# Optimization experiments

Measured on AMD Instinct MI355X. Metric: run time of the kernel, lower is better.

The kernel has to match this reference:

```python
import jax, jax.numpy as jnp
import numpy as np

H = 200
W = 200
SH = 2.0  # h / h_meters = 200/100
SW = 2.0
THRESH = 0.05   # opacity prune threshold
CHUNK = 128     # gaussians per scan step
EPS_T = 1e-4    # 3DGS transmittance early-stop
ALPHA_MIN = 1.0 / 255.0


def _rasterize(means3D, colors, opac, cov3D):
    """Orthographic BEV 3D-Gaussian-splat rasterization for one sample.
    means3D (N,3), colors (N,d), opac (N,1), cov3D (N,6) packed [xx,xy,xz,yy,yz,zz].
    Returns (d, H, W) image. Depth is identically 0 under the BEV view matrix,
    so compositing order is the input order (stable), matching the CUDA sort.
    """
    N, d = colors.shape
    P = H * W
    # pixel centers, row-major flatten: p = y*W + x
    gy, gx = jnp.meshgrid(jnp.arange(H, dtype=jnp.float32),
                          jnp.arange(W, dtype=jnp.float32), indexing='ij')
    pxf = gx.reshape(-1)
    pyf = gy.reshape(-1)

    # project means with full_proj_transform: u = -sh*y + H/2, v = -sw*x + W/2
    u = -SH * means3D[:, 1] + H / 2.0
    v = -SW * means3D[:, 0] + W / 2.0

    # 2D covariance: W2 @ Cov3D @ W2^T + 0.3*I with W2 = [[0,sh,0],[sw,0,0]]
    a = SH * SH * cov3D[:, 3] + 0.3   # var along image x (from Sigma_yy)
    c = SW * SW * cov3D[:, 0] + 0.3   # var along image y (from Sigma_xx)
    b = SH * SW * cov3D[:, 1]
    det = a * c - b * b
    valid = det > 0.0
    det_s = jnp.where(valid, det, 1.0)
    conA = c / det_s
    conB = b / det_s   # power uses +conB*dx*dy (conic.y = -b/det in CUDA)
    conC = a / det_s

    # fold pruning mask (opacity threshold) and validity into opacity
    op = jnp.where((opac[:, 0] > THRESH) & valid, opac[:, 0], 0.0)

    K = N // CHUNK
    chunks = tuple(t.reshape(K, CHUNK, *t.shape[1:])
                   for t in (u, v, conA, conB, conC, op, colors))

    def body(carry, ch):
        img, T = carry  # img (P,d), T (P,)
        u_, v_, A_, B_, C_, op_, col_ = ch
        dx = u_[:, None] - pxf[None, :]          # (C,P)
        dy = v_[:, None] - pyf[None, :]
        power = -0.5 * (A_[:, None] * dx * dx + C_[:, None] * dy * dy) \
                + B_[:, None] * dx * dy
        alpha = jnp.minimum(0.99, op_[:, None] * jnp.exp(jnp.minimum(power, 0.0)))
        # CUDA skips power>0 and alpha < 1/255
        alpha = jnp.where((power > 0.0) | (alpha < ALPHA_MIN), 0.0, alpha)
        # early termination: skip gaussian i (and all after) once T would drop < 1e-4
        T_incl = T[None, :] * jnp.cumprod(1.0 - alpha, axis=0)
        alpha = jnp.where(T_incl < EPS_T, 0.0, alpha)
        cp = jnp.cumprod(1.0 - alpha, axis=0)    # inclusive products
        T_excl = jnp.concatenate([jnp.ones((1, P), dtype=cp.dtype), cp[:-1]], axis=0)
        wgt = alpha * T_excl * T[None, :]        # (C,P)
        img = img + jnp.einsum('cp,cd->pd', wgt, col_)
        T = T * cp[-1]
        return (img, T), None

    img0 = jnp.zeros((P, d), dtype=colors.dtype)
    T0 = jnp.ones((P,), dtype=colors.dtype)
    (img, T), _ = jax.lax.scan(body, (img0, T0), chunks)
    # background is zeros -> no bg term; reshape to (d, H, W)
    return img.reshape(H, W, d).transpose(2, 0, 1)


def setup_inputs() -> dict:
    key = jax.random.key(0)
    k1, k2, k3, k4 = jax.random.split(key, 4)
    B, N, D = 2, 1024, 32
    features = jax.random.normal(k1, (B, N, D), dtype=jnp.float32)
    # BEV covers +/-50m; scale positions so most gaussians land on the canvas
    means3D = jax.random.normal(k2, (B, N, 3), dtype=jnp.float32) * 20.0
    cov3D = jax.random.uniform(k3, (B, N, 6), dtype=jnp.float32)
    opacities = jax.random.uniform(k4, (B, N, 1), dtype=jnp.float32)
    return {"features": features, "means3D": means3D,
            "cov3D": cov3D, "opacities": opacities}


def reference(features, means3D, cov3D, opacities):
    bev = jax.vmap(_rasterize)(means3D, features, opacities, cov3D)  # (B,d,H,W)
    mask = opacities[..., 0] > THRESH
    mean_count = mask.astype(jnp.float32).sum(axis=1).mean()
    return bev, mean_count
```

## Files before the change

### kernel.cpp

```cpp
#include <hip/hip_runtime.h>


#define HH 200
#define WW 200
#define DD 32
#define NG 1024
#define BB 2
#define OUT_IMG (BB*DD*HH*WW)
#define NW 4
#define SEGG (NG/NW)
#define NGRP (SEGG/64)

__global__ __launch_bounds__(64*NW) void render_kernel(
    const float* __restrict__ feats,
    const float* __restrict__ means,
    const float* __restrict__ cov,
    const float* __restrict__ opac,
    float* __restrict__ out)
{
    __shared__ float su[NW][64], sv[NW][64], sA[NW][64], sB[NW][64],
                     sC[NW][64], sop[NW][64], spl[NW][64];
    __shared__ int   sg[NW][64];
    __shared__ float4 simg[NW][64][8];
    __shared__ float sT[NW][64];
    __shared__ float wsum[NW];

    const int b    = blockIdx.z;
    const int tid  = threadIdx.x;
    const int lane = tid & 63;
    const int wid  = tid >> 6;
    const int px   = blockIdx.x*8 + (lane & 7);
    const int py   = blockIdx.y*8 + (lane >> 3);
    const float pxf = (float)px, pyf = (float)py;
    const float cx  = blockIdx.x*8 + 3.5f;
    const float cy  = blockIdx.y*8 + 3.5f;

    const float* __restrict__ featsB = feats + (size_t)b * NG * DD;
    const int gB = b * NG;

    float4 acc[8];
#pragma unroll
    for (int j = 0; j < 8; ++j) acc[j] = make_float4(0.f,0.f,0.f,0.f);
    float T = 1.f, P = 1.f;
    bool skip = false;

    for (int k = 0; k < NGRP; ++k) {
        const int gl = wid*SEGG + k*64 + lane;
        const int g  = gB + gl;
        const float o  = opac[g];
        const float c0 = cov[g*6+0], c1 = cov[g*6+1], c3 = cov[g*6+3];
        const float av = 4.f*c3 + 0.3f;
        const float cv = 4.f*c0 + 0.3f;
        const float bv = 4.f*c1;
        const float det = av*cv - bv*bv;
        bool flag = false;
        float u=0.f, v=0.f, A=0.f, Bc=0.f, Cc=0.f, pl=0.f;
        if (o > 0.05f && det > 0.f) {
            const float inv = 1.f/det;
            A = cv*inv; Bc = bv*inv; Cc = av*inv;
            u = -2.f*means[g*3+1] + 100.f;
            v = -2.f*means[g*3+0] + 100.f;
            pl = -__logf(255.f*o);
            const float qmax = -2.f*pl;
            const float htr = 0.5f*(A+Cc), hdf = 0.5f*(A-Cc);
            const float lmin = htr - sqrtf(hdf*hdf + Bc*Bc);
            const float r = sqrtf(qmax/lmin) + 0.5f;
            flag = (fabsf(u - cx) <= 3.5f + r) && (fabsf(v - cy) <= 3.5f + r);
        }
        const unsigned long long mask = __ballot(flag);
        const int m = (int)__popcll(mask);
        __syncthreads();
        if (flag) {
            const int pos = (int)__popcll(mask & ((1ull << lane) - 1ull));
            su[wid][pos]=u;  sv[wid][pos]=v;  sA[wid][pos]=A;  sB[wid][pos]=Bc;
            sC[wid][pos]=Cc; sop[wid][pos]=o; spl[wid][pos]=pl; sg[wid][pos]=gl;
        }
        __syncthreads();

        if (!skip) {
            for (int i = 0; i < m; ++i) {
                const float dx = su[wid][i] - pxf;
                const float dy = sv[wid][i] - pyf;
                const float pw = fmaf(sB[wid][i], dx*dy,
                                      -0.5f*(sA[wid][i]*dx*dx + sC[wid][i]*dy*dy));
                if (pw > 0.f) continue;
                if (pw < spl[wid][i] - 1e-3f) continue;
                const float alpha = fminf(0.99f, sop[wid][i] * __expf(pw));
                if (alpha < (1.f/255.f)) continue;
                const float om = 1.f - alpha;
                const float tp = T * P;
                if (tp * om < 1e-4f) { skip = true; break; }
                const float w = alpha * tp;
                const float4* __restrict__ col =
                    (const float4*)(featsB + (size_t)sg[wid][i] * DD);
#pragma unroll
                for (int j = 0; j < 8; ++j) {
                    const float4 c4 = col[j];
                    acc[j].x = fmaf(w, c4.x, acc[j].x);
                    acc[j].y = fmaf(w, c4.y, acc[j].y);
                    acc[j].z = fmaf(w, c4.z, acc[j].z);
                    acc[j].w = fmaf(w, c4.w, acc[j].w);
                }
                P *= om;
            }
        }
        if (k & 1) { T *= P; P = 1.f; skip = false; }
    }

    sT[wid][lane] = T;
#pragma unroll
    for (int j = 0; j < 8; ++j)
        simg[wid][lane][(j + lane) & 7] = acc[j];
    __syncthreads();

    {
        const int p   = tid & 63;
        const int grp = tid >> 6;
        const float t0 = sT[0][p], t1 = sT[1][p], t2 = sT[2][p];
        const float pf1 = t0, pf2 = t0*t1, pf3 = pf2*t2;
        const int ppx = blockIdx.x*8 + (p & 7);
        const int ppy = blockIdx.y*8 + (p >> 3);
        const size_t base = (size_t)b * DD * (HH*WW) + (size_t)ppy * WW + ppx;
#pragma unroll
        for (int q = 0; q < 2; ++q) {
            const int c4 = grp*2 + q;
            const int slot = (c4 + p) & 7;
            const float4 r0 = simg[0][p][slot];
            const float4 r1 = simg[1][p][slot];
            const float4 r2 = simg[2][p][slot];
            const float4 r3 = simg[3][p][slot];
            float4 ov;
            ov.x = fmaf(pf3, r3.x, fmaf(pf2, r2.x, fmaf(pf1, r1.x, r0.x)));
            ov.y = fmaf(pf3, r3.y, fmaf(pf2, r2.y, fmaf(pf1, r1.y, r0.y)));
            ov.z = fmaf(pf3, r3.z, fmaf(pf2, r2.z, fmaf(pf1, r1.z, r0.z)));
            ov.w = fmaf(pf3, r3.w, fmaf(pf2, r2.w, fmaf(pf1, r1.w, r0.w)));
            out[base + (size_t)(c4*4+0)*(HH*WW)] = ov.x;
            out[base + (size_t)(c4*4+1)*(HH*WW)] = ov.y;
            out[base + (size_t)(c4*4+2)*(HH*WW)] = ov.z;
            out[base + (size_t)(c4*4+3)*(HH*WW)] = ov.w;
        }
    }

    if (blockIdx.x == 0 && blockIdx.y == 0 && b == 0) {
        float s = 0.f;
        for (int i = tid; i < BB*NG; i += 64*NW)
            s += (opac[i] > 0.05f) ? 1.f : 0.f;
#pragma unroll
        for (int off = 32; off > 0; off >>= 1)
            s += __shfl_down(s, off, 64);
        if (lane == 0) wsum[wid] = s;
        __syncthreads();
        if (tid == 0)
            out[OUT_IMG] = (wsum[0]+wsum[1]+wsum[2]+wsum[3]) * (1.f/(float)BB);
    }
}

extern "C" void kernel_launch(void* const* d_in, const int* in_sizes, int n_in,
                              void* d_out, int out_size, void* d_ws, size_t ws_size,
                              hipStream_t stream) {
    const float* feats = (const float*)d_in[0];
    const float* means = (const float*)d_in[1];
    const float* cvr   = (const float*)d_in[2];
    const float* opc   = (const float*)d_in[3];
    float* out = (float*)d_out;

    render_kernel<<<dim3(WW/8, HH/8, BB), dim3(64*NW), 0, stream>>>(
        feats, means, cvr, opc, out);
}
```

Before: 77.47 us.

## Split gaussians across eight waves per tile and merge with tree reduction

Each 8x8 pixel tile now uses eight wavefronts instead of four, so each wave handles 128 gaussians. That halves the serial compositing loop per wave. The per-wave partial images are combined front-to-back through a three-level shared-memory tree reduction that carries the transmittance products. Per-pair early termination is replaced by a per-wave running transmittance, and the gaussian index is made wave-uniform with readfirstlane so the color loads can use scalar addressing. In exchange, blocks get larger, there are more barriers, and early termination within a wave's segment no longer sees the transmittance from earlier waves, so wasted work can grow.

```diff
diff --git a/kernel.cpp b/kernel.cpp
--- a/kernel.cpp
+++ b/kernel.cpp
@@ -7,7 +7,7 @@
 #define NG 1024
 #define BB 2
 #define OUT_IMG (BB*DD*HH*WW)
-#define NW 4
+#define NW 8
 #define SEGG (NG/NW)
 #define NGRP (SEGG/64)
 
@@ -20,10 +20,10 @@
 {
     __shared__ float su[NW][64], sv[NW][64], sA[NW][64], sB[NW][64],
                      sC[NW][64], sop[NW][64], spl[NW][64];
-    __shared__ int   sg[NW][64];
-    __shared__ float4 simg[NW][64][8];
-    __shared__ float sT[NW][64];
-    __shared__ float wsum[NW];
+    __shared__ int   sg_[NW][64];
+    __shared__ float4 slab[4][64][8];
+    __shared__ float  slabT[4][64];
+    __shared__ float  wsum[NW];
 
     const int b    = blockIdx.z;
     const int tid  = threadIdx.x;
@@ -41,7 +41,7 @@
     float4 acc[8];
 #pragma unroll
     for (int j = 0; j < 8; ++j) acc[j] = make_float4(0.f,0.f,0.f,0.f);
-    float T = 1.f, P = 1.f;
+    float T = 1.f;
     bool skip = false;
 
     for (int k = 0; k < NGRP; ++k) {
@@ -73,7 +73,7 @@
         if (flag) {
             const int pos = (int)__popcll(mask & ((1ull << lane) - 1ull));
             su[wid][pos]=u;  sv[wid][pos]=v;  sA[wid][pos]=A;  sB[wid][pos]=Bc;
-            sC[wid][pos]=Cc; sop[wid][pos]=o; spl[wid][pos]=pl; sg[wid][pos]=gl;
+            sC[wid][pos]=Cc; sop[wid][pos]=o; spl[wid][pos]=pl; sg_[wid][pos]=gl;
         }
         __syncthreads();
 
@@ -88,11 +88,11 @@
                 const float alpha = fminf(0.99f, sop[wid][i] * __expf(pw));
                 if (alpha < (1.f/255.f)) continue;
                 const float om = 1.f - alpha;
-                const float tp = T * P;
-                if (tp * om < 1e-4f) { skip = true; break; }
-                const float w = alpha * tp;
+                if (T * om < 1e-4f) { skip = true; break; }
+                const float w = alpha * T;
+                const int gi = __builtin_amdgcn_readfirstlane(sg_[wid][i]);
                 const float4* __restrict__ col =
-                    (const float4*)(featsB + (size_t)sg[wid][i] * DD);
+                    (const float4*)(featsB + (size_t)gi * DD);
 #pragma unroll
                 for (int j = 0; j < 8; ++j) {
                     const float4 c4 = col[j];
@@ -101,44 +101,56 @@
                     acc[j].z = fmaf(w, c4.z, acc[j].z);
                     acc[j].w = fmaf(w, c4.w, acc[j].w);
                 }
-                P *= om;
+                T *= om;
             }
         }
-        if (k & 1) { T *= P; P = 1.f; skip = false; }
     }
 
-    sT[wid][lane] = T;
+    float Tl = T;
 #pragma unroll
-    for (int j = 0; j < 8; ++j)
-        simg[wid][lane][(j + lane) & 7] = acc[j];
+    for (int phase = 0; phase < 3; ++phase) {
+        const int step = 1 << phase;
+        const int mod  = 2*step - 1;
+        const bool storer = (wid & mod) == step;
+        const bool merger = (wid & mod) == 0 && wid + step < NW;
+        __syncthreads();
+        if (storer) {
+            const int s = wid >> (phase+1);
+#pragma unroll
+            for (int j = 0; j < 8; ++j)
+                slab[s][lane][(j + lane) & 7] = acc[j];
+            slabT[s][lane] = Tl;
+        }
+        __syncthreads();
+        if (merger) {
+            const int s = (wid + step) >> (phase+1);
+            const float Th = slabT[s][lane];
+#pragma unroll
+            for (int j = 0; j < 8; ++j) {
+                const float4 r = slab[s][lane][(j + lane) & 7];
+                acc[j].x = fmaf(Tl, r.x, acc[j].x);
+                acc[j].y = fmaf(Tl, r.y, acc[j].y);
+                acc[j].z = fmaf(Tl, r.z, acc[j].z);
+                acc[j].w = fmaf(Tl, r.w, acc[j].w);
+            }
+            Tl *= Th;
+        }
+    }
+
     __syncthreads();
-
+    if (wid == 0) {
+#pragma unroll
+        for (int j = 0; j < 8; ++j)
+            slab[0][lane][(j + lane) & 7] = acc[j];
+    }
+    __syncthreads();
     {
-        const int p   = tid & 63;
-        const int grp = tid >> 6;
-        const float t0 = sT[0][p], t1 = sT[1][p], t2 = sT[2][p];
-        const float pf1 = t0, pf2 = t0*t1, pf3 = pf2*t2;
-        const int ppx = blockIdx.x*8 + (p & 7);
-        const int ppy = blockIdx.y*8 + (p >> 3);
-        const size_t base = (size_t)b * DD * (HH*WW) + (size_t)ppy * WW + ppx;
-#pragma unroll
-        for (int q = 0; q < 2; ++q) {
-            const int c4 = grp*2 + q;
-            const int slot = (c4 + p) & 7;
-            const float4 r0 = simg[0][p][slot];
-            const float4 r1 = simg[1][p][slot];
-            const float4 r2 = simg[2][p][slot];
-            const float4 r3 = simg[3][p][slot];
-            float4 ov;
-            ov.x = fmaf(pf3, r3.x, fmaf(pf2, r2.x, fmaf(pf1, r1.x, r0.x)));
-            ov.y = fmaf(pf3, r3.y, fmaf(pf2, r2.y, fmaf(pf1, r1.y, r0.y)));
-            ov.z = fmaf(pf3, r3.z, fmaf(pf2, r2.z, fmaf(pf1, r1.z, r0.z)));
-            ov.w = fmaf(pf3, r3.w, fmaf(pf2, r2.w, fmaf(pf1, r1.w, r0.w)));
-            out[base + (size_t)(c4*4+0)*(HH*WW)] = ov.x;
-            out[base + (size_t)(c4*4+1)*(HH*WW)] = ov.y;
-            out[base + (size_t)(c4*4+2)*(HH*WW)] = ov.z;
-            out[base + (size_t)(c4*4+3)*(HH*WW)] = ov.w;
-        }
+        const size_t base = (size_t)b * DD * (HH*WW) + (size_t)py * WW + px;
+        const float4 ov = slab[0][lane][(wid + lane) & 7];
+        out[base + (size_t)(wid*4+0)*(HH*WW)] = ov.x;
+        out[base + (size_t)(wid*4+1)*(HH*WW)] = ov.y;
+        out[base + (size_t)(wid*4+2)*(HH*WW)] = ov.z;
+        out[base + (size_t)(wid*4+3)*(HH*WW)] = ov.w;
     }
 
     if (blockIdx.x == 0 && blockIdx.y == 0 && b == 0) {
@@ -150,8 +162,12 @@
             s += __shfl_down(s, off, 64);
         if (lane == 0) wsum[wid] = s;
         __syncthreads();
-        if (tid == 0)
-            out[OUT_IMG] = (wsum[0]+wsum[1]+wsum[2]+wsum[3]) * (1.f/(float)BB);
+        if (tid == 0) {
+            float t = 0.f;
+#pragma unroll
+            for (int wv = 0; wv < NW; ++wv) t += wsum[wv];
+            out[OUT_IMG] = t * (1.f/(float)BB);
+        }
     }
 }
 
```

After: 77.61 us. No clear change (+0.2%).
